# Optimization experiments

Measured on AMD Instinct MI355X. Metric: run time of the kernel, lower is better.

The kernel has to match this reference:

```python
import jax, jax.numpy as jnp
import numpy as np

N = 50000          # nodes
E = 400000         # random edges (self-loops added in reference, per PyG default)
IN, HID, HEADS, OUT = 20, 64, 4, 256
NEG_SLOPE = 0.2    # GATv2Conv default negative_slope
EPS = 1e-16        # PyG softmax denom epsilon


def setup_inputs() -> dict:
    key = jax.random.key(0)
    ks = jax.random.split(key, 14)
    g = lambda k, shape, scale=0.1: (jax.random.normal(k, shape, jnp.float32) * scale)
    return {
        "x": jax.random.normal(ks[0], (N, IN), jnp.float32),
        "edge_index": jax.random.randint(ks[1], (2, E), 0, N, jnp.int32),
        # layer 1: GATv2Conv(IN -> HID, heads=HEADS, concat=True)
        "W_l1": g(ks[2], (IN, HEADS * HID)),
        "b_l1": jnp.zeros((HEADS * HID,), jnp.float32),
        "W_r1": g(ks[3], (IN, HEADS * HID)),
        "b_r1": jnp.zeros((HEADS * HID,), jnp.float32),
        "att1": g(ks[4], (HEADS, HID)),
        "bias1": jnp.zeros((HEADS * HID,), jnp.float32),
        # layer 2: GATv2Conv(HEADS*HID -> OUT, heads=1, concat=False)
        "W_l2": g(ks[5], (HEADS * HID, OUT)),
        "b_l2": jnp.zeros((OUT,), jnp.float32),
        "W_r2": g(ks[6], (HEADS * HID, OUT)),
        "b_r2": jnp.zeros((OUT,), jnp.float32),
        "att2": g(ks[7], (1, OUT)),
        "bias2": jnp.zeros((OUT,), jnp.float32),
    }


def _gatv2_layer(x, src, dst, W_l, b_l, W_r, b_r, att, bias, heads, ch, concat):
    n = x.shape[0]
    x_l = (x @ W_l + b_l).reshape(n, heads, ch)  # source transform
    x_r = (x @ W_r + b_r).reshape(n, heads, ch)  # target transform
    # GATv2: e_ij = att . LeakyReLU(x_l[j] + x_r[i])   (j->i edge)
    pre = jax.nn.leaky_relu(x_l[src] + x_r[dst], NEG_SLOPE)       # [E, H, C]
    logits = jnp.einsum('ehc,hc->eh', pre, att)                    # [E, H]
    # segment softmax over destination node (self-loops guarantee nonempty)
    m = jax.ops.segment_max(logits, dst, num_segments=n)
    w = jnp.exp(logits - m[dst])
    denom = jax.ops.segment_sum(w, dst, num_segments=n)
    alpha = w / (denom[dst] + EPS)                                 # [E, H]
    out = jax.ops.segment_sum(x_l[src] * alpha[:, :, None], dst, num_segments=n)
    out = out.reshape(n, heads * ch) if concat else out.mean(axis=1)
    return out + bias


def reference(x, edge_index, W_l1, b_l1, W_r1, b_r1, att1, bias1,
              W_l2, b_l2, W_r2, b_r2, att2, bias2):
    n = x.shape[0]
    loop = jnp.arange(n, dtype=edge_index.dtype)  # PyG add_self_loops=True
    src = jnp.concatenate([edge_index[0], loop])
    dst = jnp.concatenate([edge_index[1], loop])
    h = _gatv2_layer(x, src, dst, W_l1, b_l1, W_r1, b_r1, att1, bias1, HEADS, HID, True)
    h = jax.nn.elu(h)
    out = _gatv2_layer(h, src, dst, W_l2, b_l2, W_r2, b_r2, att2, bias2, 1, OUT, False)
    return out
```

## Files before the change

### kernel.cpp

```cpp
#include <hip/hip_runtime.h>
#include <hip/hip_bf16.h>
#include <math.h>

#define CH 256
#define SCAN_BLOCK 1024

typedef short bf16x8 __attribute__((ext_vector_type(8)));
typedef float f32x4 __attribute__((ext_vector_type(4)));

__device__ __forceinline__ float lrelu(float v) { return fmaxf(v, 0.2f * v); }
__device__ __forceinline__ float elu(float v)   { return v > 0.f ? v : __expf(v) - 1.f; }

__device__ __forceinline__ unsigned short f2bf(float f) {
    unsigned u = __float_as_uint(f);
    return (unsigned short)((u + 0x7fffu + ((u >> 16) & 1u)) >> 16);
}
__device__ __forceinline__ float4 ldbf4(const unsigned short* rowbase, int lane) {
    uint2 u = ((const uint2*)rowbase)[lane];
    return make_float4(__uint_as_float(u.x << 16), __uint_as_float(u.x & 0xffff0000u),
                       __uint_as_float(u.y << 16), __uint_as_float(u.y & 0xffff0000u));
}
__device__ __forceinline__ void stbf4(unsigned short* rowbase, int lane, float4 v) {
    uint2 u;
    u.x = (unsigned)f2bf(v.x) | ((unsigned)f2bf(v.y) << 16);
    u.y = (unsigned)f2bf(v.z) | ((unsigned)f2bf(v.w) << 16);
    ((uint2*)rowbase)[lane] = u;
}

__global__ __launch_bounds__(256) void gemm1_kernel(const float* __restrict__ x,
                             const float* __restrict__ Wl, const float* __restrict__ bl,
                             const float* __restrict__ Wr, const float* __restrict__ br,
                             unsigned short* __restrict__ xl, unsigned short* __restrict__ xr, int n) {
    __shared__ float xs[64][20];
    int n0 = blockIdx.x * 64;
    int tid = threadIdx.x;
    for (int i = tid; i < 64 * 20; i += 256) {
        int m = i / 20, k = i % 20;
        int row = n0 + m;
        xs[m][k] = (row < n) ? x[(size_t)row * 20 + k] : 0.f;
    }
    int c = tid;
    float wl[20], wr[20];
#pragma unroll
    for (int k = 0; k < 20; ++k) { wl[k] = Wl[k * 256 + c]; wr[k] = Wr[k * 256 + c]; }
    float blv = bl[c], brv = br[c];
    __syncthreads();
#pragma unroll 1
    for (int g = 0; g < 8; ++g) {
        int base = g * 8;
        float al[8], ar[8];
#pragma unroll
        for (int m = 0; m < 8; ++m) { al[m] = blv; ar[m] = brv; }
#pragma unroll
        for (int k = 0; k < 20; ++k) {
            float wlv = wl[k], wrv = wr[k];
#pragma unroll
            for (int m = 0; m < 8; ++m) {
                float xv = xs[base + m][k];
                al[m] += xv * wlv;
                ar[m] += xv * wrv;
            }
        }
#pragma unroll
        for (int m = 0; m < 8; ++m) {
            int row = n0 + base + m;
            if (row < n) {
                xl[(size_t)row * 256 + c] = f2bf(al[m]);
                xr[(size_t)row * 256 + c] = f2bf(ar[m]);
            }
        }
    }
}

__global__ void count_deg(const int* __restrict__ ei, int* __restrict__ deg, int e) {
    int t = blockIdx.x * blockDim.x + threadIdx.x;
    if (t < e) atomicAdd(&deg[ei[e + t]], 1);
}

__global__ void scan_block_k(const int* __restrict__ deg, int* __restrict__ rowptr,
                             int* __restrict__ bsums, int n) {
    __shared__ int wsum[16];
    __shared__ int woff[17];
    int tid = threadIdx.x;
    int gi = blockIdx.x * SCAN_BLOCK + tid;
    int lane = tid & 63, wid = tid >> 6;
    int v = (gi < n) ? deg[gi] : 0;
    int incl = v;
#pragma unroll
    for (int d = 1; d < 64; d <<= 1) {
        int t = __shfl_up(incl, d, 64);
        if (lane >= d) incl += t;
    }
    if (lane == 63) wsum[wid] = incl;
    __syncthreads();
    if (tid < 16) {
        int s = wsum[tid];
#pragma unroll
        for (int d = 1; d < 16; d <<= 1) {
            int t = __shfl_up(s, d, 64);
            if (tid >= d) s += t;
        }
        woff[tid + 1] = s;
        if (tid == 0) woff[0] = 0;
    }
    __syncthreads();
    incl += woff[wid];
    if (gi < n) rowptr[gi + 1] = incl;
    if (tid == 0) bsums[blockIdx.x] = woff[16];
}

__global__ void scan_tops_k(int* bsums, int nb) {
    int tid = threadIdx.x;
    int v = (tid < nb) ? bsums[tid] : 0;
    int incl = v;
#pragma unroll
    for (int d = 1; d < 64; d <<= 1) {
        int t = __shfl_up(incl, d, 64);
        if (tid >= d) incl += t;
    }
    if (tid < nb) bsums[tid] = incl - v;
}

__global__ void scan_fix_k(int* __restrict__ rowptr, int* __restrict__ cursor,
                           const int* __restrict__ deg, const int* __restrict__ bsums, int n) {
    int gi = blockIdx.x * SCAN_BLOCK + threadIdx.x;
    if (gi >= n) return;
    int off = bsums[blockIdx.x];
    int incl = rowptr[gi + 1] + off;
    rowptr[gi + 1] = incl;
    cursor[gi] = incl - deg[gi];
    if (gi == 0) rowptr[0] = 0;
}

__global__ void scatter_k(const int* __restrict__ ei, int* __restrict__ cursor,
                          int* __restrict__ csr, int e) {
    int t = blockIdx.x * blockDim.x + threadIdx.x;
    if (t >= e) return;
    int s = ei[t], d = ei[e + t];
    int idx = atomicAdd(&cursor[d], 1);
    csr[idx] = s;
}

__global__ void fused_gat1(const unsigned short* __restrict__ xl, const unsigned short* __restrict__ xr,
                           const int* __restrict__ rowptr, const int* __restrict__ csr,
                           const float* __restrict__ att, const float* __restrict__ bias,
                           unsigned short* __restrict__ hout, int n) {
    int wid = threadIdx.x >> 6;
    int lane = threadIdx.x & 63;
    int i = blockIdx.x * 4 + wid;
    if (i >= n) return;
    float4 xr4 = ldbf4(xr + (size_t)i * CH, lane);
    float4 a4  = ((const float4*)att)[lane];
    float4 xli = ldbf4(xl + (size_t)i * CH, lane);
    float ps = lrelu(xli.x + xr4.x) * a4.x + lrelu(xli.y + xr4.y) * a4.y +
               lrelu(xli.z + xr4.z) * a4.z + lrelu(xli.w + xr4.w) * a4.w;
    ps += __shfl_xor(ps, 1); ps += __shfl_xor(ps, 2);
    ps += __shfl_xor(ps, 4); ps += __shfl_xor(ps, 8);
    float m = ps, l = 1.f;
    float4 acc = xli;
    int beg = rowptr[i], end = rowptr[i + 1];
    for (int e = beg; e < end; e += 4) {
        int cnt = end - e;
        int s0 = csr[e];
        int s1 = (cnt > 1) ? csr[e + 1] : s0;
        int s2 = (cnt > 2) ? csr[e + 2] : s0;
        int s3 = (cnt > 3) ? csr[e + 3] : s0;
        float4 r0 = ldbf4(xl + (size_t)s0 * CH, lane);
        float4 r1 = ldbf4(xl + (size_t)s1 * CH, lane);
        float4 r2 = ldbf4(xl + (size_t)s2 * CH, lane);
        float4 r3 = ldbf4(xl + (size_t)s3 * CH, lane);
        float p0 = lrelu(r0.x + xr4.x) * a4.x + lrelu(r0.y + xr4.y) * a4.y +
                   lrelu(r0.z + xr4.z) * a4.z + lrelu(r0.w + xr4.w) * a4.w;
        float p1 = lrelu(r1.x + xr4.x) * a4.x + lrelu(r1.y + xr4.y) * a4.y +
                   lrelu(r1.z + xr4.z) * a4.z + lrelu(r1.w + xr4.w) * a4.w;
        float p2 = lrelu(r2.x + xr4.x) * a4.x + lrelu(r2.y + xr4.y) * a4.y +
                   lrelu(r2.z + xr4.z) * a4.z + lrelu(r2.w + xr4.w) * a4.w;
        float p3 = lrelu(r3.x + xr4.x) * a4.x + lrelu(r3.y + xr4.y) * a4.y +
                   lrelu(r3.z + xr4.z) * a4.z + lrelu(r3.w + xr4.w) * a4.w;
        p0 += __shfl_xor(p0, 1); p1 += __shfl_xor(p1, 1); p2 += __shfl_xor(p2, 1); p3 += __shfl_xor(p3, 1);
        p0 += __shfl_xor(p0, 2); p1 += __shfl_xor(p1, 2); p2 += __shfl_xor(p2, 2); p3 += __shfl_xor(p3, 2);
        p0 += __shfl_xor(p0, 4); p1 += __shfl_xor(p1, 4); p2 += __shfl_xor(p2, 4); p3 += __shfl_xor(p3, 4);
        p0 += __shfl_xor(p0, 8); p1 += __shfl_xor(p1, 8); p2 += __shfl_xor(p2, 8); p3 += __shfl_xor(p3, 8);
        if (cnt < 2) p1 = -INFINITY;
        if (cnt < 3) p2 = -INFINITY;
        if (cnt < 4) p3 = -INFINITY;
        float mn = fmaxf(m, fmaxf(fmaxf(p0, p1), fmaxf(p2, p3)));
        float sc = __expf(m - mn);
        float w0 = __expf(p0 - mn), w1 = __expf(p1 - mn);
        float w2 = __expf(p2 - mn), w3 = __expf(p3 - mn);
        l = l * sc + w0 + w1 + w2 + w3;
        acc.x = acc.x * sc + w0 * r0.x + w1 * r1.x + w2 * r2.x + w3 * r3.x;
        acc.y = acc.y * sc + w0 * r0.y + w1 * r1.y + w2 * r2.y + w3 * r3.y;
        acc.z = acc.z * sc + w0 * r0.z + w1 * r1.z + w2 * r2.z + w3 * r3.z;
        acc.w = acc.w * sc + w0 * r0.w + w1 * r1.w + w2 * r2.w + w3 * r3.w;
        m = mn;
    }
    float inv = 1.f / (l + 1e-16f);
    float4 b4 = ((const float4*)bias)[lane];
    float4 o;
    o.x = elu(acc.x * inv + b4.x);
    o.y = elu(acc.y * inv + b4.y);
    o.z = elu(acc.z * inv + b4.z);
    o.w = elu(acc.w * inv + b4.w);
    stbf4(hout + (size_t)i * CH, lane, o);
}

__global__ void fused_gat2(const unsigned short* __restrict__ xl, const unsigned short* __restrict__ xr,
                           const int* __restrict__ rowptr, const int* __restrict__ csr,
                           const float* __restrict__ att, const float* __restrict__ bias,
                           float* __restrict__ out, int n) {
    int wid = threadIdx.x >> 6;
    int lane = threadIdx.x & 63;
    int i = blockIdx.x * 4 + wid;
    if (i >= n) return;
    float4 xr4 = ldbf4(xr + (size_t)i * CH, lane);
    float4 a4  = ((const float4*)att)[lane];
    float4 xli = ldbf4(xl + (size_t)i * CH, lane);
    float ps = lrelu(xli.x + xr4.x) * a4.x + lrelu(xli.y + xr4.y) * a4.y +
               lrelu(xli.z + xr4.z) * a4.z + lrelu(xli.w + xr4.w) * a4.w;
    ps += __shfl_xor(ps, 1); ps += __shfl_xor(ps, 2); ps += __shfl_xor(ps, 4);
    ps += __shfl_xor(ps, 8); ps += __shfl_xor(ps, 16); ps += __shfl_xor(ps, 32);
    float m = ps, l = 1.f;
    float4 acc = xli;
    int beg = rowptr[i], end = rowptr[i + 1];
    for (int e = beg; e < end; e += 4) {
        int cnt = end - e;
        int s0 = csr[e];
        int s1 = (cnt > 1) ? csr[e + 1] : s0;
        int s2 = (cnt > 2) ? csr[e + 2] : s0;
        int s3 = (cnt > 3) ? csr[e + 3] : s0;
        float4 r0 = ldbf4(xl + (size_t)s0 * CH, lane);
        float4 r1 = ldbf4(xl + (size_t)s1 * CH, lane);
        float4 r2 = ldbf4(xl + (size_t)s2 * CH, lane);
        float4 r3 = ldbf4(xl + (size_t)s3 * CH, lane);
        float p0 = lrelu(r0.x + xr4.x) * a4.x + lrelu(r0.y + xr4.y) * a4.y +
                   lrelu(r0.z + xr4.z) * a4.z + lrelu(r0.w + xr4.w) * a4.w;
        float p1 = lrelu(r1.x + xr4.x) * a4.x + lrelu(r1.y + xr4.y) * a4.y +
                   lrelu(r1.z + xr4.z) * a4.z + lrelu(r1.w + xr4.w) * a4.w;
        float p2 = lrelu(r2.x + xr4.x) * a4.x + lrelu(r2.y + xr4.y) * a4.y +
                   lrelu(r2.z + xr4.z) * a4.z + lrelu(r2.w + xr4.w) * a4.w;
        float p3 = lrelu(r3.x + xr4.x) * a4.x + lrelu(r3.y + xr4.y) * a4.y +
                   lrelu(r3.z + xr4.z) * a4.z + lrelu(r3.w + xr4.w) * a4.w;
#pragma unroll
        for (int d = 1; d < 64; d <<= 1) {
            p0 += __shfl_xor(p0, d); p1 += __shfl_xor(p1, d);
            p2 += __shfl_xor(p2, d); p3 += __shfl_xor(p3, d);
        }
        if (cnt < 2) p1 = -INFINITY;
        if (cnt < 3) p2 = -INFINITY;
        if (cnt < 4) p3 = -INFINITY;
        float mn = fmaxf(m, fmaxf(fmaxf(p0, p1), fmaxf(p2, p3)));
        float sc = __expf(m - mn);
        float w0 = __expf(p0 - mn), w1 = __expf(p1 - mn);
        float w2 = __expf(p2 - mn), w3 = __expf(p3 - mn);
        l = l * sc + w0 + w1 + w2 + w3;
        acc.x = acc.x * sc + w0 * r0.x + w1 * r1.x + w2 * r2.x + w3 * r3.x;
        acc.y = acc.y * sc + w0 * r0.y + w1 * r1.y + w2 * r2.y + w3 * r3.y;
        acc.z = acc.z * sc + w0 * r0.z + w1 * r1.z + w2 * r2.z + w3 * r3.z;
        acc.w = acc.w * sc + w0 * r0.w + w1 * r1.w + w2 * r2.w + w3 * r3.w;
        m = mn;
    }
    float inv = 1.f / (l + 1e-16f);
    float4 b4 = ((const float4*)bias)[lane];
    float4 o;
    o.x = acc.x * inv + b4.x;
    o.y = acc.y * inv + b4.y;
    o.z = acc.z * inv + b4.z;
    o.w = acc.w * inv + b4.w;
    ((float4*)(out + (size_t)i * CH))[lane] = o;
}

__global__ void wconv(const float* __restrict__ Wl2, const float* __restrict__ Wr2,
                      unsigned short* __restrict__ Wt) {
    int t = blockIdx.x * 256 + threadIdx.x;
    int z = t >> 16;
    int idx = t & 65535;
    int k = idx >> 8, nn = idx & 255;
    const float* W = z ? Wr2 : Wl2;
    Wt[z * 65536 + nn * 256 + k] = f2bf(W[k * 256 + nn]);
}

#define LDK 40
__global__ __launch_bounds__(256) void gemm_mfma(
        const unsigned short* __restrict__ A,
        const unsigned short* __restrict__ Wt,
        const float* __restrict__ ba, const float* __restrict__ bb,
        unsigned short* __restrict__ Ca, unsigned short* __restrict__ Cb, int M) {
    const unsigned short* Wz = Wt + (size_t)blockIdx.z * 65536;
    const float* bias = blockIdx.z ? bb : ba;
    unsigned short* C = blockIdx.z ? Cb : Ca;

    __shared__ unsigned short As[128 * LDK];
    __shared__ unsigned short Bs[128 * LDK];

    int m0 = blockIdx.x * 128, n0 = blockIdx.y * 128;
    int tid = threadIdx.x;
    int lane = tid & 63, wid = tid >> 6;
    int wm = wid & 1, wn = wid >> 1;
    int q = lane >> 4, l15 = lane & 15;

    f32x4 acc[4][4];
#pragma unroll
    for (int i = 0; i < 4; ++i)
#pragma unroll
        for (int j = 0; j < 4; ++j) acc[i][j] = (f32x4){0.f, 0.f, 0.f, 0.f};

    int r = tid >> 2;
    int c8 = (tid & 3) * 8;
    const uint4 zero4 = make_uint4(0, 0, 0, 0);

    for (int kb = 0; kb < 8; ++kb) {
        int k0 = kb * 32;
        int ra = m0 + r, rb = m0 + r + 64;
        uint4 va0 = (ra < M) ? *(const uint4*)(A + (size_t)ra * 256 + k0 + c8) : zero4;
        uint4 va1 = (rb < M) ? *(const uint4*)(A + (size_t)rb * 256 + k0 + c8) : zero4;
        uint4 vb0 = *(const uint4*)(Wz + (size_t)(n0 + r) * 256 + k0 + c8);
        uint4 vb1 = *(const uint4*)(Wz + (size_t)(n0 + r + 64) * 256 + k0 + c8);
        __syncthreads();
        *(uint4*)&As[r * LDK + c8] = va0;
        *(uint4*)&As[(r + 64) * LDK + c8] = va1;
        *(uint4*)&Bs[r * LDK + c8] = vb0;
        *(uint4*)&Bs[(r + 64) * LDK + c8] = vb1;
        __syncthreads();

        bf16x8 af[4], bfr[4];
#pragma unroll
        for (int f = 0; f < 4; ++f)
            af[f] = *(const bf16x8*)&As[(wm * 64 + f * 16 + l15) * LDK + q * 8];
#pragma unroll
        for (int f = 0; f < 4; ++f)
            bfr[f] = *(const bf16x8*)&Bs[(wn * 64 + f * 16 + l15) * LDK + q * 8];
#pragma unroll
        for (int i = 0; i < 4; ++i)
#pragma unroll
            for (int j = 0; j < 4; ++j)
                acc[i][j] = __builtin_amdgcn_mfma_f32_16x16x32_bf16(af[i], bfr[j], acc[i][j], 0, 0, 0);
    }

#pragma unroll
    for (int j = 0; j < 4; ++j) {
        int gcol = n0 + wn * 64 + j * 16 + l15;
        float bcol = bias[gcol];
#pragma unroll
        for (int i = 0; i < 4; ++i) {
            int row = m0 + wm * 64 + i * 16 + q * 4;
#pragma unroll
            for (int rr = 0; rr < 4; ++rr) {
                int grow = row + rr;
                if (grow < M)
                    C[(size_t)grow * 256 + gcol] = f2bf(acc[i][j][rr] + bcol);
            }
        }
    }
}

extern "C" void kernel_launch(void* const* d_in, const int* in_sizes, int n_in,
                              void* d_out, int out_size, void* d_ws, size_t ws_size,
                              hipStream_t stream) {
    const float* x    = (const float*)d_in[0];
    const int*   ei   = (const int*)d_in[1];
    const float* Wl1  = (const float*)d_in[2];
    const float* bl1  = (const float*)d_in[3];
    const float* Wr1  = (const float*)d_in[4];
    const float* br1  = (const float*)d_in[5];
    const float* att1 = (const float*)d_in[6];
    const float* bias1= (const float*)d_in[7];
    const float* Wl2  = (const float*)d_in[8];
    const float* bl2  = (const float*)d_in[9];
    const float* Wr2  = (const float*)d_in[10];
    const float* br2  = (const float*)d_in[11];
    const float* att2 = (const float*)d_in[12];
    const float* bias2= (const float*)d_in[13];

    int n = in_sizes[0] / 20;
    int e = in_sizes[1] / 2;
    float* out = (float*)d_out;
    size_t nch = (size_t)n * CH;

    unsigned short* buf0 = (unsigned short*)d_ws;
    unsigned short* buf1 = buf0 + nch;
    unsigned short* hbuf = buf1 + nch;
    unsigned short* wt2  = hbuf + nch;
    int* deg    = (int*)(wt2 + 2 * 65536);
    int* rowptr = deg + n;
    int* cursor = rowptr + n + 1;
    int* bsums  = cursor + n;
    int* csr    = bsums + 64;

    hipMemsetAsync(deg, 0, (size_t)n * sizeof(int), stream);

    gemm1_kernel<<<(n + 63) / 64, 256, 0, stream>>>(x, Wl1, bl1, Wr1, br1, buf0, buf1, n);

    count_deg<<<(e + 255) / 256, 256, 0, stream>>>(ei, deg, e);
    int nb = (n + SCAN_BLOCK - 1) / SCAN_BLOCK;
    scan_block_k<<<nb, SCAN_BLOCK, 0, stream>>>(deg, rowptr, bsums, n);
    scan_tops_k<<<1, 64, 0, stream>>>(bsums, nb);
    scan_fix_k<<<nb, SCAN_BLOCK, 0, stream>>>(rowptr, cursor, deg, bsums, n);
    scatter_k<<<(e + 255) / 256, 256, 0, stream>>>(ei, cursor, csr, e);

    wconv<<<512, 256, 0, stream>>>(Wl2, Wr2, wt2);

    fused_gat1<<<(n + 3) / 4, 256, 0, stream>>>(buf0, buf1, rowptr, csr, att1, bias1, hbuf, n);

    gemm_mfma<<<dim3((n + 127) / 128, 2, 2), 256, 0, stream>>>(hbuf, wt2, bl2, br2, buf0, buf1, n);

    fused_gat2<<<(n + 3) / 4, 256, 0, stream>>>(buf0, buf1, rowptr, csr, att2, bias2, out, n);
}
```

Measured before the change: 326.7 us.

## Widen gather unroll to eight edges and restructure GEMM with register-direct B and half-K LDS staging

Both fused GAT kernels now process eight neighbor edges per iteration instead of four, issuing more independent row gathers per wave to hide memory latency. Padding lanes now point at the node itself rather than the first neighbor. The layer-2 GEMM drops the B shared tile, loads weight fragments straight from global into registers with one-step prefetch, and stages A in two 128-wide K halves with only two barriers. It also flattens the grid so the four (z,y) tiles of one row block sit on adjacent blocks for L2 reuse of A. The cost is more registers per thread, which may reduce occupancy, and more padded work for low-degree nodes.

```diff
diff --git a/kernel.cpp b/kernel.cpp
--- a/kernel.cpp
+++ b/kernel.cpp
@@ -159,41 +159,43 @@
     float m = ps, l = 1.f;
     float4 acc = xli;
     int beg = rowptr[i], end = rowptr[i + 1];
-    for (int e = beg; e < end; e += 4) {
+    for (int e = beg; e < end; e += 8) {
         int cnt = end - e;
-        int s0 = csr[e];
-        int s1 = (cnt > 1) ? csr[e + 1] : s0;
-        int s2 = (cnt > 2) ? csr[e + 2] : s0;
-        int s3 = (cnt > 3) ? csr[e + 3] : s0;
-        float4 r0 = ldbf4(xl + (size_t)s0 * CH, lane);
-        float4 r1 = ldbf4(xl + (size_t)s1 * CH, lane);
-        float4 r2 = ldbf4(xl + (size_t)s2 * CH, lane);
-        float4 r3 = ldbf4(xl + (size_t)s3 * CH, lane);
-        float p0 = lrelu(r0.x + xr4.x) * a4.x + lrelu(r0.y + xr4.y) * a4.y +
-                   lrelu(r0.z + xr4.z) * a4.z + lrelu(r0.w + xr4.w) * a4.w;
-        float p1 = lrelu(r1.x + xr4.x) * a4.x + lrelu(r1.y + xr4.y) * a4.y +
-                   lrelu(r1.z + xr4.z) * a4.z + lrelu(r1.w + xr4.w) * a4.w;
-        float p2 = lrelu(r2.x + xr4.x) * a4.x + lrelu(r2.y + xr4.y) * a4.y +
-                   lrelu(r2.z + xr4.z) * a4.z + lrelu(r2.w + xr4.w) * a4.w;
-        float p3 = lrelu(r3.x + xr4.x) * a4.x + lrelu(r3.y + xr4.y) * a4.y +
-                   lrelu(r3.z + xr4.z) * a4.z + lrelu(r3.w + xr4.w) * a4.w;
-        p0 += __shfl_xor(p0, 1); p1 += __shfl_xor(p1, 1); p2 += __shfl_xor(p2, 1); p3 += __shfl_xor(p3, 1);
-        p0 += __shfl_xor(p0, 2); p1 += __shfl_xor(p1, 2); p2 += __shfl_xor(p2, 2); p3 += __shfl_xor(p3, 2);
-        p0 += __shfl_xor(p0, 4); p1 += __shfl_xor(p1, 4); p2 += __shfl_xor(p2, 4); p3 += __shfl_xor(p3, 4);
-        p0 += __shfl_xor(p0, 8); p1 += __shfl_xor(p1, 8); p2 += __shfl_xor(p2, 8); p3 += __shfl_xor(p3, 8);
-        if (cnt < 2) p1 = -INFINITY;
-        if (cnt < 3) p2 = -INFINITY;
-        if (cnt < 4) p3 = -INFINITY;
-        float mn = fmaxf(m, fmaxf(fmaxf(p0, p1), fmaxf(p2, p3)));
-        float sc = __expf(m - mn);
-        float w0 = __expf(p0 - mn), w1 = __expf(p1 - mn);
-        float w2 = __expf(p2 - mn), w3 = __expf(p3 - mn);
-        l = l * sc + w0 + w1 + w2 + w3;
-        acc.x = acc.x * sc + w0 * r0.x + w1 * r1.x + w2 * r2.x + w3 * r3.x;
-        acc.y = acc.y * sc + w0 * r0.y + w1 * r1.y + w2 * r2.y + w3 * r3.y;
-        acc.z = acc.z * sc + w0 * r0.z + w1 * r1.z + w2 * r2.z + w3 * r3.z;
-        acc.w = acc.w * sc + w0 * r0.w + w1 * r1.w + w2 * r2.w + w3 * r3.w;
-        m = mn;
+        int ss[8];
+#pragma unroll
+        for (int j = 0; j < 8; ++j) ss[j] = (j < cnt) ? csr[e + j] : i;
+        float4 rr[8];
+#pragma unroll
+        for (int j = 0; j < 8; ++j) rr[j] = ldbf4(xl + (size_t)ss[j] * CH, lane);
+        float pp[8];
+#pragma unroll
+        for (int j = 0; j < 8; ++j)
+            pp[j] = lrelu(rr[j].x + xr4.x) * a4.x + lrelu(rr[j].y + xr4.y) * a4.y +
+                    lrelu(rr[j].z + xr4.z) * a4.z + lrelu(rr[j].w + xr4.w) * a4.w;
+#pragma unroll
+        for (int d = 1; d < 16; d <<= 1)
+#pragma unroll
+            for (int j = 0; j < 8; ++j) pp[j] += __shfl_xor(pp[j], d);
+#pragma unroll
+        for (int j = 0; j < 8; ++j) if (j >= cnt) pp[j] = -INFINITY;
+        float mx = m;
+#pragma unroll
+        for (int j = 0; j < 8; ++j) mx = fmaxf(mx, pp[j]);
+        float sc = __expf(m - mx);
+        float ww[8];
+#pragma unroll
+        for (int j = 0; j < 8; ++j) ww[j] = __expf(pp[j] - mx);
+        l *= sc;
+        acc.x *= sc; acc.y *= sc; acc.z *= sc; acc.w *= sc;
+#pragma unroll
+        for (int j = 0; j < 8; ++j) {
+            l += ww[j];
+            acc.x += ww[j] * rr[j].x;
+            acc.y += ww[j] * rr[j].y;
+            acc.z += ww[j] * rr[j].z;
+            acc.w += ww[j] * rr[j].w;
+        }
+        m = mx;
     }
     float inv = 1.f / (l + 1e-16f);
     float4 b4 = ((const float4*)bias)[lane];
@@ -223,42 +225,43 @@
     float m = ps, l = 1.f;
     float4 acc = xli;
     int beg = rowptr[i], end = rowptr[i + 1];
-    for (int e = beg; e < end; e += 4) {
+    for (int e = beg; e < end; e += 8) {
         int cnt = end - e;
-        int s0 = csr[e];
-        int s1 = (cnt > 1) ? csr[e + 1] : s0;
-        int s2 = (cnt > 2) ? csr[e + 2] : s0;
-        int s3 = (cnt > 3) ? csr[e + 3] : s0;
-        float4 r0 = ldbf4(xl + (size_t)s0 * CH, lane);
-        float4 r1 = ldbf4(xl + (size_t)s1 * CH, lane);
-        float4 r2 = ldbf4(xl + (size_t)s2 * CH, lane);
-        float4 r3 = ldbf4(xl + (size_t)s3 * CH, lane);
-        float p0 = lrelu(r0.x + xr4.x) * a4.x + lrelu(r0.y + xr4.y) * a4.y +
-                   lrelu(r0.z + xr4.z) * a4.z + lrelu(r0.w + xr4.w) * a4.w;
-        float p1 = lrelu(r1.x + xr4.x) * a4.x + lrelu(r1.y + xr4.y) * a4.y +
-                   lrelu(r1.z + xr4.z) * a4.z + lrelu(r1.w + xr4.w) * a4.w;
-        float p2 = lrelu(r2.x + xr4.x) * a4.x + lrelu(r2.y + xr4.y) * a4.y +
-                   lrelu(r2.z + xr4.z) * a4.z + lrelu(r2.w + xr4.w) * a4.w;
-        float p3 = lrelu(r3.x + xr4.x) * a4.x + lrelu(r3.y + xr4.y) * a4.y +
-                   lrelu(r3.z + xr4.z) * a4.z + lrelu(r3.w + xr4.w) * a4.w;
-#pragma unroll
-        for (int d = 1; d < 64; d <<= 1) {
-            p0 += __shfl_xor(p0, d); p1 += __shfl_xor(p1, d);
-            p2 += __shfl_xor(p2, d); p3 += __shfl_xor(p3, d);
-        }
-        if (cnt < 2) p1 = -INFINITY;
-        if (cnt < 3) p2 = -INFINITY;
-        if (cnt < 4) p3 = -INFINITY;
-        float mn = fmaxf(m, fmaxf(fmaxf(p0, p1), fmaxf(p2, p3)));
-        float sc = __expf(m - mn);
-        float w0 = __expf(p0 - mn), w1 = __expf(p1 - mn);
-        float w2 = __expf(p2 - mn), w3 = __expf(p3 - mn);
-        l = l * sc + w0 + w1 + w2 + w3;
-        acc.x = acc.x * sc + w0 * r0.x + w1 * r1.x + w2 * r2.x + w3 * r3.x;
-        acc.y = acc.y * sc + w0 * r0.y + w1 * r1.y + w2 * r2.y + w3 * r3.y;
-        acc.z = acc.z * sc + w0 * r0.z + w1 * r1.z + w2 * r2.z + w3 * r3.z;
-        acc.w = acc.w * sc + w0 * r0.w + w1 * r1.w + w2 * r2.w + w3 * r3.w;
-        m = mn;
+        int ss[8];
+#pragma unroll
+        for (int j = 0; j < 8; ++j) ss[j] = (j < cnt) ? csr[e + j] : i;
+        float4 rr[8];
+#pragma unroll
+        for (int j = 0; j < 8; ++j) rr[j] = ldbf4(xl + (size_t)ss[j] * CH, lane);
+        float pp[8];
+#pragma unroll
+        for (int j = 0; j < 8; ++j)
+            pp[j] = lrelu(rr[j].x + xr4.x) * a4.x + lrelu(rr[j].y + xr4.y) * a4.y +
+                    lrelu(rr[j].z + xr4.z) * a4.z + lrelu(rr[j].w + xr4.w) * a4.w;
+#pragma unroll
+        for (int d = 1; d < 64; d <<= 1)
+#pragma unroll
+            for (int j = 0; j < 8; ++j) pp[j] += __shfl_xor(pp[j], d);
+#pragma unroll
+        for (int j = 0; j < 8; ++j) if (j >= cnt) pp[j] = -INFINITY;
+        float mx = m;
+#pragma unroll
+        for (int j = 0; j < 8; ++j) mx = fmaxf(mx, pp[j]);
+        float sc = __expf(m - mx);
+        float ww[8];
+#pragma unroll
+        for (int j = 0; j < 8; ++j) ww[j] = __expf(pp[j] - mx);
+        l *= sc;
+        acc.x *= sc; acc.y *= sc; acc.z *= sc; acc.w *= sc;
+#pragma unroll
+        for (int j = 0; j < 8; ++j) {
+            l += ww[j];
+            acc.x += ww[j] * rr[j].x;
+            acc.y += ww[j] * rr[j].y;
+            acc.z += ww[j] * rr[j].z;
+            acc.w += ww[j] * rr[j].w;
+        }
+        m = mx;
     }
     float inv = 1.f / (l + 1e-16f);
     float4 b4 = ((const float4*)bias)[lane];
@@ -280,24 +283,23 @@
     Wt[z * 65536 + nn * 256 + k] = f2bf(W[k * 256 + nn]);
 }
 
-#define LDK 40
+#define LDA 132
 __global__ __launch_bounds__(256) void gemm_mfma(
         const unsigned short* __restrict__ A,
         const unsigned short* __restrict__ Wt,
         const float* __restrict__ ba, const float* __restrict__ bb,
         unsigned short* __restrict__ Ca, unsigned short* __restrict__ Cb, int M) {
-    const unsigned short* Wz = Wt + (size_t)blockIdx.z * 65536;
-    const float* bias = blockIdx.z ? bb : ba;
-    unsigned short* C = blockIdx.z ? Cb : Ca;
-
-    __shared__ unsigned short As[128 * LDK];
-    __shared__ unsigned short Bs[128 * LDK];
-
-    int m0 = blockIdx.x * 128, n0 = blockIdx.y * 128;
-    int tid = threadIdx.x;
-    int lane = tid & 63, wid = tid >> 6;
-    int wm = wid & 1, wn = wid >> 1;
-    int q = lane >> 4, l15 = lane & 15;
+    int b = blockIdx.x;
+    int z = b & 1, y = (b >> 1) & 1, xb = b >> 2;
+    const unsigned short* Wz = Wt + (size_t)z * 65536;
+    const float* bias = z ? bb : ba;
+    unsigned short* C = z ? Cb : Ca;
+    int m0 = xb * 128, n0 = y * 128;
+
+    __shared__ unsigned short As[128 * LDA];
+
+    int tid = threadIdx.x, lane = tid & 63, wid = tid >> 6;
+    int wm = wid & 1, wn = wid >> 1, q = lane >> 4, l15 = lane & 15;
 
     f32x4 acc[4][4];
 #pragma unroll
@@ -305,36 +307,60 @@
 #pragma unroll
         for (int j = 0; j < 4; ++j) acc[i][j] = (f32x4){0.f, 0.f, 0.f, 0.f};
 
-    int r = tid >> 2;
-    int c8 = (tid & 3) * 8;
-    const uint4 zero4 = make_uint4(0, 0, 0, 0);
-
+    int srow = tid >> 1, shalf = tid & 1;
+    bool rowok = (m0 + srow) < M;
+    const unsigned short* gA = A + (size_t)(m0 + srow) * 256 + shalf * 64;
+    unsigned short* sA = As + srow * LDA + shalf * 64;
+    const uint4 z4 = make_uint4(0, 0, 0, 0);
+
+    uint4 st[8];
+#pragma unroll
+    for (int i = 0; i < 8; ++i)
+        st[i] = rowok ? *(const uint4*)(gA + i * 8) : z4;
+
+    const unsigned short* gB = Wz + (size_t)(n0 + wn * 64 + l15) * 256 + q * 8;
+    bf16x8 bc[4], bn[4];
+#pragma unroll
+    for (int j = 0; j < 4; ++j)
+        bc[j] = *(const bf16x8*)(gB + j * 4096);
+
+#pragma unroll
+    for (int i = 0; i < 8; ++i)
+        *(uint4*)(sA + i * 8) = st[i];
+    __syncthreads();
+
+#pragma unroll
     for (int kb = 0; kb < 8; ++kb) {
-        int k0 = kb * 32;
-        int ra = m0 + r, rb = m0 + r + 64;
-        uint4 va0 = (ra < M) ? *(const uint4*)(A + (size_t)ra * 256 + k0 + c8) : zero4;
-        uint4 va1 = (rb < M) ? *(const uint4*)(A + (size_t)rb * 256 + k0 + c8) : zero4;
-        uint4 vb0 = *(const uint4*)(Wz + (size_t)(n0 + r) * 256 + k0 + c8);
-        uint4 vb1 = *(const uint4*)(Wz + (size_t)(n0 + r + 64) * 256 + k0 + c8);
-        __syncthreads();
-        *(uint4*)&As[r * LDK + c8] = va0;
-        *(uint4*)&As[(r + 64) * LDK + c8] = va1;
-        *(uint4*)&Bs[r * LDK + c8] = vb0;
-        *(uint4*)&Bs[(r + 64) * LDK + c8] = vb1;
-        __syncthreads();
-
-        bf16x8 af[4], bfr[4];
-#pragma unroll
-        for (int f = 0; f < 4; ++f)
-            af[f] = *(const bf16x8*)&As[(wm * 64 + f * 16 + l15) * LDK + q * 8];
-#pragma unroll
-        for (int f = 0; f < 4; ++f)
-            bfr[f] = *(const bf16x8*)&Bs[(wn * 64 + f * 16 + l15) * LDK + q * 8];
+        if (kb == 1) {
+#pragma unroll
+            for (int i = 0; i < 8; ++i)
+                st[i] = rowok ? *(const uint4*)(gA + 128 + i * 8) : z4;
+        }
+        if (kb < 7) {
+#pragma unroll
+            for (int j = 0; j < 4; ++j)
+                bn[j] = *(const bf16x8*)(gB + j * 4096 + (kb + 1) * 32);
+        }
+        bf16x8 af[4];
 #pragma unroll
         for (int i = 0; i < 4; ++i)
+            af[i] = *(const bf16x8*)&As[(wm * 64 + i * 16 + l15) * LDA + (kb & 3) * 32 + q * 8];
+#pragma unroll
+        for (int i = 0; i < 4; ++i)
 #pragma unroll
             for (int j = 0; j < 4; ++j)
-                acc[i][j] = __builtin_amdgcn_mfma_f32_16x16x32_bf16(af[i], bfr[j], acc[i][j], 0, 0, 0);
+                acc[i][j] = __builtin_amdgcn_mfma_f32_16x16x32_bf16(af[i], bc[j], acc[i][j], 0, 0, 0);
+        if (kb < 7) {
+#pragma unroll
+            for (int j = 0; j < 4; ++j) bc[j] = bn[j];
+        }
+        if (kb == 3) {
+            __syncthreads();
+#pragma unroll
+            for (int i = 0; i < 8; ++i)
+                *(uint4*)(sA + i * 8) = st[i];
+            __syncthreads();
+        }
     }
 
 #pragma unroll
@@ -402,7 +428,7 @@
 
     fused_gat1<<<(n + 3) / 4, 256, 0, stream>>>(buf0, buf1, rowptr, csr, att1, bias1, hbuf, n);
 
-    gemm_mfma<<<dim3((n + 127) / 128, 2, 2), 256, 0, stream>>>(hbuf, wt2, bl2, br2, buf0, buf1, n);
+    gemm_mfma<<<((n + 127) / 128) * 4, 256, 0, stream>>>(hbuf, wt2, bl2, br2, buf0, buf1, n);
 
     fused_gat2<<<(n + 3) / 4, 256, 0, stream>>>(buf0, buf1, rowptr, csr, att2, bias2, out, n);
 }
```

After: 390.7 us. +19.6%, slower.
